# Kernel optimization log

Hardware: AMD Instinct MI355X
Metric: run time of the kernel (lower is better)

Reference implementation:

```python
import jax, jax.numpy as jnp
import numpy as np

MODEL_DIM = 1024
NUM_HEADS = 16
K_DIM = MODEL_DIM // NUM_HEADS


def setup_inputs() -> dict:
    key = jax.random.key(0)
    kx, kw1, kw2 = jax.random.split(key, 3)
    B, L, D = 4, 2048, MODEL_DIM
    x = jax.random.normal(kx, (B, L, D), dtype=jnp.float32)
    # nn.Linear(D, 3D, bias=False): y = x @ W^T; store transposed form [D, 3D]
    scale1 = 1.0 / np.sqrt(D)
    Wqkv = jax.random.uniform(kw1, (D, 3 * D), dtype=jnp.float32, minval=-scale1, maxval=scale1)
    Wout = jax.random.uniform(kw2, (D, D), dtype=jnp.float32, minval=-scale1, maxval=scale1)
    return {"x": x, "Wqkv": Wqkv, "Wout": Wout}


def reference(x, Wqkv, Wout):
    B, L, D = x.shape
    H, Kd = NUM_HEADS, K_DIM
    qkv = x @ Wqkv  # [B, L, 3D]
    q, k, v = jnp.split(qkv, 3, axis=-1)

    def heads(t):  # [B, L, D] -> [B, H, L, Kd]
        return t.reshape(B, L, H, Kd).transpose(0, 2, 1, 3)

    qh, kh, vh = heads(q), heads(k), heads(v)
    scores = jnp.einsum('bhqd,bhkd->bhqk', qh, kh) / jnp.sqrt(jnp.float32(Kd))
    causal = jnp.triu(jnp.ones((L, L), dtype=bool), k=1)  # True above diagonal
    scores = jnp.where(causal, -jnp.inf, scores)
    probs = jax.nn.softmax(scores, axis=-1)
    attended = jnp.einsum('bhqk,bhkd->bhqd', probs, vh)
    concatted = attended.transpose(0, 2, 1, 3).reshape(B, L, D)
    # dropout is identity in eval mode
    return concatted @ Wout
```

## Files before the change

kernel.cpp:

```cpp
#include <hip/hip_runtime.h>

typedef unsigned short u16;
typedef unsigned int   u32;
typedef __bf16   bf16x8 __attribute__((ext_vector_type(8)));
typedef float    f32x4  __attribute__((ext_vector_type(4)));
typedef u16      u16x4  __attribute__((ext_vector_type(4)));
typedef u16      u16x8  __attribute__((ext_vector_type(8)));
typedef u32      u32x2  __attribute__((ext_vector_type(2)));
typedef u32      u32x4  __attribute__((ext_vector_type(4)));

#if __has_builtin(__builtin_amdgcn_exp2f)
#define EXP2(x) __builtin_amdgcn_exp2f(x)
#else
#define EXP2(x) exp2f(x)
#endif

__device__ __forceinline__ u16 f2bf(float f) {
    unsigned u = __float_as_uint(f);
    u += 0x7FFFu + ((u >> 16) & 1u);
    return (u16)(u >> 16);
}

__device__ __forceinline__ u32 pack_bf16(float a, float b) {
#if __has_builtin(__builtin_amdgcn_cvt_pk_bf16_f32)
    typedef __bf16 bf16x2 __attribute__((ext_vector_type(2)));
    bf16x2 r = __builtin_amdgcn_cvt_pk_bf16_f32(a, b);
    return __builtin_bit_cast(u32, r);
#else
    return (u32)f2bf(a) | ((u32)f2bf(b) << 16);
#endif
}

__device__ __forceinline__ void async_copy16(const u16* g, u16* l) {
    __builtin_amdgcn_global_load_lds(
        (const __attribute__((address_space(1))) unsigned*)g,
        (__attribute__((address_space(3))) unsigned*)l, 16, 0, 0);
}

__device__ __forceinline__ bf16x8 lds_frag(const u16* p) {
    return *(const bf16x8*)p;
}

__device__ __forceinline__ void permlane32_swap(u32& a, u32& b) {
    asm("v_permlane32_swap_b32 %0, %1" : "+v"(a), "+v"(b));
}
__device__ __forceinline__ void permlane16_swap(u32& a, u32& b) {
    asm("v_permlane16_swap_b32 %0, %1" : "+v"(a), "+v"(b));
}

__global__ __launch_bounds__(256) void prep(const float* __restrict__ x,
                                            const float* __restrict__ Wqkv,
                                            const float* __restrict__ Wout,
                                            u16* __restrict__ xb,
                                            u16* __restrict__ wqkv_t,
                                            u16* __restrict__ wout_t) {
    __shared__ u16 t[64 * 72];
    const int bid = blockIdx.x;
    const int tid = threadIdx.x;

    if (bid >= 1024) {
        size_t i = ((size_t)(bid - 1024) * 256 + tid) * 8;
        float4 v0 = *(const float4*)(x + i);
        float4 v1 = *(const float4*)(x + i + 4);
        u16x8 o = { f2bf(v0.x), f2bf(v0.y), f2bf(v0.z), f2bf(v0.w),
                    f2bf(v1.x), f2bf(v1.y), f2bf(v1.z), f2bf(v1.w) };
        *(u16x8*)(xb + i) = o;
        return;
    }

    const float* W;  u16* Wt;  int Kd, Nd, n0, k0;
    if (bid < 768) { W = Wqkv; Wt = wqkv_t; Kd = 1024; Nd = 3072;
                     n0 = (bid % 48) * 64; k0 = (bid / 48) * 64; }
    else           { W = Wout; Wt = wout_t; Kd = 1024; Nd = 1024;
                     n0 = ((bid - 768) % 16) * 64; k0 = ((bid - 768) / 16) * 64; }
#pragma unroll
    for (int i = 0; i < 4; ++i) {
        int lin = i * 256 + tid;
        int kr = lin >> 4, nc = (lin & 15) << 2;
        float4 v = *(const float4*)(W + (size_t)(k0 + kr) * Nd + n0 + nc);
        u16x4 o = { f2bf(v.x), f2bf(v.y), f2bf(v.z), f2bf(v.w) };
        *(u16x4*)&t[kr * 72 + nc] = o;
    }
    __syncthreads();
#pragma unroll
    for (int i = 0; i < 2; ++i) {
        int lin = i * 256 + tid;
        int nr = lin >> 3, kc = (lin & 7) << 3;
        u16x8 o;
#pragma unroll
        for (int jj = 0; jj < 8; ++jj) o[jj] = t[(kc + jj) * 72 + nr];
        *(u16x8*)(Wt + (size_t)(n0 + nr) * Kd + k0 + kc) = o;
    }
}

__global__ __launch_bounds__(256) void gemm_qkv(const u16* __restrict__ A,
                                                const u16* __restrict__ Bt,
                                                u16* __restrict__ outb,
                                                int K, int N) {
    __shared__ u16 As[2][128 * 32];
    __shared__ u16 Bs[2][128 * 32];
    const int tid = threadIdx.x;
    const int lane = tid & 63;
    const int wv = tid >> 6;
    const int wr = (wv >> 1) * 64;
    const int wc = (wv & 1) * 64;
    const int qd = lane >> 4;
    const int c  = lane & 15;
    const int m0 = blockIdx.y * 128;
    const int n0 = blockIdx.x * 128;

    const int srow = tid >> 2;
    const int sg = ((tid & 3) ^ ((srow >> 1) & 3)) << 3;

    const u16* Ag0 = A  + (size_t)(m0 +      srow) * K + sg;
    const u16* Ag1 = A  + (size_t)(m0 + 64 + srow) * K + sg;
    const u16* Bg0 = Bt + (size_t)(n0 +      srow) * K + sg;
    const u16* Bg1 = Bt + (size_t)(n0 + 64 + srow) * K + sg;

    const u32 fsw = (qd ^ ((c >> 1) & 3)) << 3;
    const u32 a_off = (wr + c) * 32 + fsw;
    const u32 b_off = (wc + c) * 32 + fsw;

    f32x4 acc[4][4] = {};

    async_copy16(Ag0, &As[0][tid * 8]);
    async_copy16(Ag1, &As[0][2048 + tid * 8]);
    async_copy16(Bg0, &Bs[0][tid * 8]);
    async_copy16(Bg1, &Bs[0][2048 + tid * 8]);

    int p = 0;
    for (int k0 = 0; k0 < K; k0 += 32) {
        __syncthreads();
        if (k0 + 32 < K) {
            const int np = p ^ 1;
            async_copy16(Ag0 + k0 + 32, &As[np][tid * 8]);
            async_copy16(Ag1 + k0 + 32, &As[np][2048 + tid * 8]);
            async_copy16(Bg0 + k0 + 32, &Bs[np][tid * 8]);
            async_copy16(Bg1 + k0 + 32, &Bs[np][2048 + tid * 8]);
        }
        bf16x8 af[4], bfr[4];
#pragma unroll
        for (int i = 0; i < 4; ++i) af[i]  = lds_frag(&As[p][a_off + i * 512]);
#pragma unroll
        for (int j = 0; j < 4; ++j) bfr[j] = lds_frag(&Bs[p][b_off + j * 512]);
#pragma unroll
        for (int i = 0; i < 4; ++i)
#pragma unroll
            for (int j = 0; j < 4; ++j)
                acc[i][j] = __builtin_amdgcn_mfma_f32_16x16x32_bf16(af[i], bfr[j], acc[i][j], 0, 0, 0);
        p ^= 1;
    }

#pragma unroll
    for (int i = 0; i < 4; ++i)
#pragma unroll
        for (int j = 0; j < 4; ++j) {
            int n = n0 + wc + j * 16 + c;
            int which = n >> 10, h = (n >> 6) & 15, kd = n & 63;
            int m_base = m0 + wr + i * 16 + qd * 4;
            int b = m_base >> 11, l0 = m_base & 2047;
            int bh = b * 16 + h;
            if (which == 2) {
                u32x2 o2;
                o2[0] = pack_bf16(acc[i][j][0], acc[i][j][1]);
                o2[1] = pack_bf16(acc[i][j][2], acc[i][j][3]);
                *(u32x2*)(outb + (size_t)(128 + bh) * 131072 + (size_t)kd * 2048 + l0) = o2;
            } else if (which == 0) {
#pragma unroll
                for (int r = 0; r < 4; ++r)
                    outb[(size_t)bh * 131072 + (size_t)(l0 + r) * 64 + kd] =
                        f2bf(acc[i][j][r] * 0.1803368801f);
            } else {
#pragma unroll
                for (int r = 0; r < 4; ++r)
                    outb[(size_t)(64 + bh) * 131072 + (size_t)(l0 + r) * 64 + kd] =
                        f2bf(acc[i][j][r]);
            }
        }
}

__global__ __launch_bounds__(256) void gemm_out(const u16* __restrict__ A,
                                                const u16* __restrict__ Bt,
                                                float* __restrict__ outf,
                                                int K, int N) {
    __shared__ u16 As[2][64 * 32];
    __shared__ u16 Bs[2][128 * 32];
    const int tid = threadIdx.x;
    const int lane = tid & 63;
    const int wv = tid >> 6;
    const int wr = (wv >> 1) * 32;
    const int wc = (wv & 1) * 64;
    const int qd = lane >> 4;
    const int c  = lane & 15;
    const int m0 = blockIdx.y * 64;
    const int n0 = blockIdx.x * 128;

    const int srow = tid >> 2;
    const int sg = ((tid & 3) ^ ((srow >> 1) & 3)) << 3;

    const u16* Ag0 = A  + (size_t)(m0 +      srow) * K + sg;
    const u16* Bg0 = Bt + (size_t)(n0 +      srow) * K + sg;
    const u16* Bg1 = Bt + (size_t)(n0 + 64 + srow) * K + sg;

    const u32 fsw = (qd ^ ((c >> 1) & 3)) << 3;
    const u32 a_off = (wr + c) * 32 + fsw;
    const u32 b_off = (wc + c) * 32 + fsw;

    f32x4 acc[2][4] = {};

    async_copy16(Ag0, &As[0][tid * 8]);
    async_copy16(Bg0, &Bs[0][tid * 8]);
    async_copy16(Bg1, &Bs[0][2048 + tid * 8]);

    int p = 0;
    for (int k0 = 0; k0 < K; k0 += 32) {
        __syncthreads();
        if (k0 + 32 < K) {
            const int np = p ^ 1;
            async_copy16(Ag0 + k0 + 32, &As[np][tid * 8]);
            async_copy16(Bg0 + k0 + 32, &Bs[np][tid * 8]);
            async_copy16(Bg1 + k0 + 32, &Bs[np][2048 + tid * 8]);
        }
        bf16x8 af[2], bfr[4];
#pragma unroll
        for (int i = 0; i < 2; ++i) af[i]  = lds_frag(&As[p][a_off + i * 512]);
#pragma unroll
        for (int j = 0; j < 4; ++j) bfr[j] = lds_frag(&Bs[p][b_off + j * 512]);
#pragma unroll
        for (int i = 0; i < 2; ++i)
#pragma unroll
            for (int j = 0; j < 4; ++j)
                acc[i][j] = __builtin_amdgcn_mfma_f32_16x16x32_bf16(af[i], bfr[j], acc[i][j], 0, 0, 0);
        p ^= 1;
    }

#pragma unroll
    for (int i = 0; i < 2; ++i)
#pragma unroll
        for (int j = 0; j < 4; ++j)
#pragma unroll
            for (int r = 0; r < 4; ++r) {
                int m = m0 + wr + i * 16 + qd * 4 + r;
                int n = n0 + wc + j * 16 + c;
                outf[(size_t)m * N + n] = acc[i][j][r];
            }
}

#define ATTN_S_AB(KSB)                                                        \
    do {                                                                      \
        _Pragma("unroll") for (int f = 0; f < 8; ++f) {                       \
            sa[f] = f32x4{-8.f, -8.f, -8.f, -8.f};                            \
            sb[f] = f32x4{-8.f, -8.f, -8.f, -8.f};                            \
        }                                                                     \
        __builtin_amdgcn_s_setprio(1);                                        \
        _Pragma("unroll") for (int ks = 0; ks < 2; ++ks) {                    \
            const u16* kp = (KSB) + kf_off[ks];                               \
            _Pragma("unroll") for (int f = 0; f < 8; ++f) {                   \
                bf16x8 kf = lds_frag(kp + f * 1024);                          \
                sa[f] = __builtin_amdgcn_mfma_f32_16x16x32_bf16(              \
                    kf, qa[ks], sa[f], 0, 0, 0);                              \
                sb[f] = __builtin_amdgcn_mfma_f32_16x16x32_bf16(              \
                    kf, qb[ks], sb[f], 0, 0, 0);                              \
            }                                                                 \
        }                                                                     \
        __builtin_amdgcn_s_setprio(0);                                        \
    } while (0)

#define ATTN_FINISH_AB(VTB, KT)                                               \
    do {                                                                      \
        if ((KT) == qt) {                                                     \
            _Pragma("unroll") for (int f = 0; f < 8; ++f)                     \
                _Pragma("unroll") for (int r = 0; r < 4; ++r) {               \
                    int key = (KT) * 128 + f * 16 + qd * 4 + r;               \
                    if (key > qa_row) sa[f][r] = -3e38f;                      \
                    if (key > qb_row) sb[f][r] = -3e38f;                      \
                }                                                             \
        }                                                                     \
        _Pragma("unroll") for (int f = 0; f < 8; ++f) {                       \
            _Pragma("unroll") for (int r = 0; r < 4; ++r) {                   \
                sa[f][r] = EXP2(sa[f][r]);                                    \
                sb[f][r] = EXP2(sb[f][r]);                                    \
            }                                                                 \
            rva += sa[f];                                                     \
            rvb += sb[f];                                                     \
        }                                                                     \
        _Pragma("unroll") for (int kc = 0; kc < 4; ++kc) {                    \
            u32 a0 = pack_bf16(sa[2 * kc][0], sa[2 * kc][1]);                 \
            u32 a1 = pack_bf16(sa[2 * kc + 1][0], sa[2 * kc + 1][1]);         \
            u32 b0 = pack_bf16(sa[2 * kc][2], sa[2 * kc][3]);                 \
            u32 b1 = pack_bf16(sa[2 * kc + 1][2], sa[2 * kc + 1][3]);         \
            permlane32_swap(a0, a1); permlane16_swap(a0, a1);                 \
            permlane32_swap(b0, b1); permlane16_swap(b0, b1);                 \
            u32x4 wpa = {a0, b0, a1, b1};                                     \
            bf16x8 pa = __builtin_bit_cast(bf16x8, wpa);                      \
            u32 c0 = pack_bf16(sb[2 * kc][0], sb[2 * kc][1]);                 \
            u32 c1 = pack_bf16(sb[2 * kc + 1][0], sb[2 * kc + 1][1]);         \
            u32 d0 = pack_bf16(sb[2 * kc][2], sb[2 * kc][3]);                 \
            u32 d1 = pack_bf16(sb[2 * kc + 1][2], sb[2 * kc + 1][3]);         \
            permlane32_swap(c0, c1); permlane16_swap(c0, c1);                 \
            permlane32_swap(d0, d1); permlane16_swap(d0, d1);                 \
            u32x4 wpb = {c0, d0, c1, d1};                                     \
            bf16x8 pb = __builtin_bit_cast(bf16x8, wpb);                      \
            const u16* vp = (VTB) + vf_off[kc];                               \
            __builtin_amdgcn_s_setprio(1);                                    \
            _Pragma("unroll") for (int jo = 0; jo < 4; ++jo) {                \
                bf16x8 vf = lds_frag(vp + jo * 2048);                         \
                acca[jo] = __builtin_amdgcn_mfma_f32_16x16x32_bf16(           \
                    vf, pa, acca[jo], 0, 0, 0);                               \
                accb[jo] = __builtin_amdgcn_mfma_f32_16x16x32_bf16(           \
                    vf, pb, accb[jo], 0, 0, 0);                               \
            }                                                                 \
            __builtin_amdgcn_s_setprio(0);                                    \
        }                                                                     \
    } while (0)

__global__ __launch_bounds__(256, 2) void attn_kernel(const u16* __restrict__ qkv,
                                                      u16* __restrict__ att) {
    __shared__ u16 Ks[2][128 * 64];
    __shared__ u16 Vt[2][64 * 128];

    const int tid = threadIdx.x;
    const int lane = tid & 63;
    const int w = tid >> 6;
    const int qd = lane >> 4;
    const int c = lane & 15;

    const int flat = blockIdx.x + 8 * blockIdx.y;
    const int bh = (flat & 7) + 8 * ((flat >> 3) & 7);
    const int bx = flat >> 6;
    const int b = bh >> 4, h = bh & 15;

    const u16* Qg = qkv + (size_t)bh * 131072;
    const u16* Kg = qkv + (size_t)(64 + bh) * 131072;
    const u16* Vg = qkv + (size_t)(128 + bh) * 131072;

    u32 kf_off[2];
#pragma unroll
    for (int ks = 0; ks < 2; ++ks)
        kf_off[ks] = c * 64 + (((ks * 4 + qd) ^ (c & 7)) << 3);
    u32 vf_off[4];
#pragma unroll
    for (int kc = 0; kc < 4; ++kc)
        vf_off[kc] = c * 128 + (((kc * 4 + qd) ^ c) << 3);

    auto issue_copy = [&](int t, u16* kd, u16* vd) {
#pragma unroll
        for (int it = 0; it < 4; ++it) {
            int lin = it * 256 + tid;
            int krw = lin >> 3, kch = lin & 7;
            int vrw = lin >> 4, vch = lin & 15;
            async_copy16(Kg + (size_t)t * 8192 + krw * 64 + ((kch ^ (krw & 7)) << 3),
                         kd + lin * 8);
            async_copy16(Vg + (size_t)t * 128 + (size_t)vrw * 2048 + ((vch ^ (vrw & 15)) << 3),
                         vd + lin * 8);
        }
    };

#pragma unroll 1
    for (int seg = 0; seg < 2; ++seg) {
        const int qt = seg ? (15 - bx) : bx;
        const int qa_row = qt * 128 + w * 32 + c;
        const int qb_row = qa_row + 16;

        bf16x8 qa[2], qb[2];
#pragma unroll
        for (int ks = 0; ks < 2; ++ks) {
            qa[ks] = *(const bf16x8*)(Qg + (size_t)qa_row * 64 + ks * 32 + qd * 8);
            qb[ks] = *(const bf16x8*)(Qg + (size_t)qb_row * 64 + ks * 32 + qd * 8);
        }

        f32x4 acca[4] = {}, accb[4] = {};
        f32x4 rva = {}, rvb = {};
        f32x4 sa[8], sb[8];

        const int nkt = qt + 1;

        __syncthreads();
        issue_copy(0, Ks[0], Vt[0]);
        __syncthreads();
        if (nkt > 1) issue_copy(1, Ks[1], Vt[1]);

#pragma unroll 1
        for (int kt = 0; kt < nkt; ++kt) {
            const int p = kt & 1;
            ATTN_S_AB(Ks[p]);
            ATTN_FINISH_AB(Vt[p], kt);
            if (kt + 1 < nkt) {
                __syncthreads();
                if (kt + 2 < nkt) issue_copy(kt + 2, Ks[p], Vt[p]);
            }
        }

        float ra = rva[0] + rva[1] + rva[2] + rva[3];
        float rb = rvb[0] + rvb[1] + rvb[2] + rvb[3];
        ra += __shfl_xor(ra, 16, 64);
        ra += __shfl_xor(ra, 32, 64);
        rb += __shfl_xor(rb, 16, 64);
        rb += __shfl_xor(rb, 32, 64);
        float ia = __builtin_amdgcn_rcpf(ra), ib = __builtin_amdgcn_rcpf(rb);
        u16* ar = att + ((size_t)b * 2048 + qa_row) * 1024 + h * 64;
        u16* br = att + ((size_t)b * 2048 + qb_row) * 1024 + h * 64;
#pragma unroll
        for (int jo = 0; jo < 4; ++jo) {
            u32x2 oa, ob;
            oa[0] = pack_bf16(acca[jo][0] * ia, acca[jo][1] * ia);
            oa[1] = pack_bf16(acca[jo][2] * ia, acca[jo][3] * ia);
            ob[0] = pack_bf16(accb[jo][0] * ib, accb[jo][1] * ib);
            ob[1] = pack_bf16(accb[jo][2] * ib, accb[jo][3] * ib);
            *(u32x2*)(ar + jo * 16 + qd * 4) = oa;
            *(u32x2*)(br + jo * 16 + qd * 4) = ob;
        }
    }
}

extern "C" void kernel_launch(void* const* d_in, const int* in_sizes, int n_in,
                              void* d_out, int out_size, void* d_ws, size_t ws_size,
                              hipStream_t stream) {
    const float* x    = (const float*)d_in[0];
    const float* Wqkv = (const float*)d_in[1];
    const float* Wout = (const float*)d_in[2];
    float* out = (float*)d_out;

    char* ws = (char*)d_ws;
    u16* x_bf   = (u16*)(ws);
    u16* wqkv_t = (u16*)(ws + 16777216);
    u16* wout_t = (u16*)(ws + 23068672);
    u16* qkv_h  = (u16*)(ws + 25165824);
    u16* att    = (u16*)(ws + 75497472);

    prep<<<dim3(5120), dim3(256), 0, stream>>>(x, Wqkv, Wout, x_bf, wqkv_t, wout_t);
    gemm_qkv<<<dim3(24, 64), dim3(256), 0, stream>>>(x_bf, wqkv_t, qkv_h, 1024, 3072);
    attn_kernel<<<dim3(8, 64), dim3(256), 0, stream>>>(qkv_h, att);
    gemm_out<<<dim3(8, 128), dim3(256), 0, stream>>>(att, wout_t, out, 1024, 1024);
}
```

Baseline: 246.2 us.

## Enlarge QKV GEMM to 256x256 tiles with 8 waves and swizzled block order

Rewrites the QKV projection GEMM to use 256x256 output tiles with 512 threads (8 waves), a BK of 64 with a double-buffered LDS ring, and explicit waitcnt/barrier scheduling with setprio around the MFMA clusters. The block index is remapped so that consecutive blocks share input tiles in the L2 cache. The aim is more data reuse per loaded tile and better overlap of global loads with MFMA work. In exchange it uses much more LDS (128KB) and more accumulator registers, which lowers occupancy and leaves only 384 blocks to spread over the CUs.

```diff
diff --git a/kernel.cpp b/kernel.cpp
--- a/kernel.cpp
+++ b/kernel.cpp
@@ -93,71 +93,136 @@
     }
 }
 
-__global__ __launch_bounds__(256) void gemm_qkv(const u16* __restrict__ A,
+__global__ __launch_bounds__(512) void gemm_qkv(const u16* __restrict__ A,
                                                 const u16* __restrict__ Bt,
                                                 u16* __restrict__ outb,
                                                 int K, int N) {
-    __shared__ u16 As[2][128 * 32];
-    __shared__ u16 Bs[2][128 * 32];
+    __shared__ u16 As[2][2][128 * 64];
+    __shared__ u16 Bs[2][2][128 * 64];
+
     const int tid = threadIdx.x;
     const int lane = tid & 63;
-    const int wv = tid >> 6;
-    const int wr = (wv >> 1) * 64;
-    const int wc = (wv & 1) * 64;
+    const int wid = tid >> 6;
+    const int wr = wid >> 2;
+    const int wc = wid & 3;
     const int qd = lane >> 4;
     const int c  = lane & 15;
-    const int m0 = blockIdx.y * 128;
-    const int n0 = blockIdx.x * 128;
-
-    const int srow = tid >> 2;
-    const int sg = ((tid & 3) ^ ((srow >> 1) & 3)) << 3;
-
-    const u16* Ag0 = A  + (size_t)(m0 +      srow) * K + sg;
-    const u16* Ag1 = A  + (size_t)(m0 + 64 + srow) * K + sg;
-    const u16* Bg0 = Bt + (size_t)(n0 +      srow) * K + sg;
-    const u16* Bg1 = Bt + (size_t)(n0 + 64 + srow) * K + sg;
-
-    const u32 fsw = (qd ^ ((c >> 1) & 3)) << 3;
-    const u32 a_off = (wr + c) * 32 + fsw;
-    const u32 b_off = (wc + c) * 32 + fsw;
-
-    f32x4 acc[4][4] = {};
-
-    async_copy16(Ag0, &As[0][tid * 8]);
-    async_copy16(Ag1, &As[0][2048 + tid * 8]);
-    async_copy16(Bg0, &Bs[0][tid * 8]);
-    async_copy16(Bg1, &Bs[0][2048 + tid * 8]);
-
-    int p = 0;
-    for (int k0 = 0; k0 < K; k0 += 32) {
-        __syncthreads();
-        if (k0 + 32 < K) {
-            const int np = p ^ 1;
-            async_copy16(Ag0 + k0 + 32, &As[np][tid * 8]);
-            async_copy16(Ag1 + k0 + 32, &As[np][2048 + tid * 8]);
-            async_copy16(Bg0 + k0 + 32, &Bs[np][tid * 8]);
-            async_copy16(Bg1 + k0 + 32, &Bs[np][2048 + tid * 8]);
-        }
+
+    const int flat = blockIdx.x;
+    const int swz  = (flat & 7) * 48 + (flat >> 3);
+    const int m0 = (swz / 12) * 256;
+    const int n0 = (swz % 12) * 256;
+
+    const u32 ch0 = (u32)((qd ^ (c & 7)) << 3);
+    const u32 ch1 = (u32)(((4 + qd) ^ (c & 7)) << 3);
+    const u32 arow = (u32)c * 64;
+    const u32 brow = ((u32)((wc & 1) * 64) + (u32)c) * 64;
+
+    auto stage = [&](int t, int slot) {
+        const int kb = t * 64;
+#pragma unroll
+        for (int it = 0; it < 4; ++it) {
+            int lin = it * 512 + tid;
+            int row = lin >> 3;
+            int sch = ((lin & 7) ^ (row & 7)) << 3;
+            async_copy16(A  + (size_t)(m0 + row) * K + kb + sch,
+                         &As[slot][0][0] + (size_t)lin * 8);
+            async_copy16(Bt + (size_t)(n0 + row) * K + kb + sch,
+                         &Bs[slot][0][0] + (size_t)lin * 8);
+        }
+    };
+
+    f32x4 acc[8][4] = {};
+
+    stage(0, 0);
+    stage(1, 1);
+    asm volatile("s_waitcnt vmcnt(8)" ::: "memory");
+    __builtin_amdgcn_s_barrier();
+
+    const int NT = K >> 6;
+#pragma unroll 1
+    for (int kt = 0; kt < NT; ++kt) {
+        const int p = kt & 1;
+        const u16* Ab = &As[p][wr][0];
+        const u16* Bb = &Bs[p][wc >> 1][0];
+
         bf16x8 af[4], bfr[4];
-#pragma unroll
-        for (int i = 0; i < 4; ++i) af[i]  = lds_frag(&As[p][a_off + i * 512]);
-#pragma unroll
-        for (int j = 0; j < 4; ++j) bfr[j] = lds_frag(&Bs[p][b_off + j * 512]);
+
+#pragma unroll
+        for (int i = 0; i < 4; ++i) af[i]  = lds_frag(Ab + arow + i * 1024 + ch0);
+#pragma unroll
+        for (int j = 0; j < 4; ++j) bfr[j] = lds_frag(Bb + brow + j * 1024 + ch0);
+        __builtin_amdgcn_s_barrier();
+        asm volatile("s_waitcnt lgkmcnt(0)" ::: "memory");
+        __builtin_amdgcn_sched_barrier(0);
+        __builtin_amdgcn_s_setprio(1);
 #pragma unroll
         for (int i = 0; i < 4; ++i)
 #pragma unroll
             for (int j = 0; j < 4; ++j)
                 acc[i][j] = __builtin_amdgcn_mfma_f32_16x16x32_bf16(af[i], bfr[j], acc[i][j], 0, 0, 0);
-        p ^= 1;
+        __builtin_amdgcn_s_setprio(0);
+        __builtin_amdgcn_s_barrier();
+
+#pragma unroll
+        for (int i = 0; i < 4; ++i) af[i] = lds_frag(Ab + arow + (4 + i) * 1024 + ch0);
+        __builtin_amdgcn_s_barrier();
+        asm volatile("s_waitcnt lgkmcnt(0)" ::: "memory");
+        __builtin_amdgcn_sched_barrier(0);
+        __builtin_amdgcn_s_setprio(1);
+#pragma unroll
+        for (int i = 0; i < 4; ++i)
+#pragma unroll
+            for (int j = 0; j < 4; ++j)
+                acc[4 + i][j] = __builtin_amdgcn_mfma_f32_16x16x32_bf16(af[i], bfr[j], acc[4 + i][j], 0, 0, 0);
+        __builtin_amdgcn_s_setprio(0);
+        __builtin_amdgcn_s_barrier();
+
+#pragma unroll
+        for (int i = 0; i < 4; ++i) af[i]  = lds_frag(Ab + arow + i * 1024 + ch1);
+#pragma unroll
+        for (int j = 0; j < 4; ++j) bfr[j] = lds_frag(Bb + brow + j * 1024 + ch1);
+        __builtin_amdgcn_s_barrier();
+        asm volatile("s_waitcnt lgkmcnt(0)" ::: "memory");
+        __builtin_amdgcn_sched_barrier(0);
+        __builtin_amdgcn_s_setprio(1);
+#pragma unroll
+        for (int i = 0; i < 4; ++i)
+#pragma unroll
+            for (int j = 0; j < 4; ++j)
+                acc[i][j] = __builtin_amdgcn_mfma_f32_16x16x32_bf16(af[i], bfr[j], acc[i][j], 0, 0, 0);
+        __builtin_amdgcn_s_setprio(0);
+        __builtin_amdgcn_s_barrier();
+
+#pragma unroll
+        for (int i = 0; i < 4; ++i) af[i] = lds_frag(Ab + arow + (4 + i) * 1024 + ch1);
+        __builtin_amdgcn_s_barrier();
+        asm volatile("s_waitcnt lgkmcnt(0)" ::: "memory");
+        __builtin_amdgcn_sched_barrier(0);
+        __builtin_amdgcn_s_setprio(1);
+#pragma unroll
+        for (int i = 0; i < 4; ++i)
+#pragma unroll
+            for (int j = 0; j < 4; ++j)
+                acc[4 + i][j] = __builtin_amdgcn_mfma_f32_16x16x32_bf16(af[i], bfr[j], acc[4 + i][j], 0, 0, 0);
+        __builtin_amdgcn_s_setprio(0);
+        __builtin_amdgcn_s_barrier();
+
+        if (kt + 2 < NT) stage(kt + 2, p);
+        if (kt + 1 < NT) {
+            if (kt + 2 < NT) asm volatile("s_waitcnt vmcnt(8)" ::: "memory");
+            else             asm volatile("s_waitcnt vmcnt(0)" ::: "memory");
+            __builtin_amdgcn_s_barrier();
+        }
     }
 
 #pragma unroll
-    for (int i = 0; i < 4; ++i)
+    for (int i = 0; i < 8; ++i)
 #pragma unroll
         for (int j = 0; j < 4; ++j) {
-            int n = n0 + wc + j * 16 + c;
+            int n = n0 + wc * 64 + j * 16 + c;
             int which = n >> 10, h = (n >> 6) & 15, kd = n & 63;
-            int m_base = m0 + wr + i * 16 + qd * 4;
+            int m_base = m0 + wr * 128 + i * 16 + qd * 4;
             int b = m_base >> 11, l0 = m_base & 2047;
             int bh = b * 16 + h;
             if (which == 2) {
@@ -429,7 +494,7 @@
     u16* att    = (u16*)(ws + 75497472);
 
     prep<<<dim3(5120), dim3(256), 0, stream>>>(x, Wqkv, Wout, x_bf, wqkv_t, wout_t);
-    gemm_qkv<<<dim3(24, 64), dim3(256), 0, stream>>>(x_bf, wqkv_t, qkv_h, 1024, 3072);
+    gemm_qkv<<<dim3(384), dim3(512), 0, stream>>>(x_bf, wqkv_t, qkv_h, 1024, 3072);
     attn_kernel<<<dim3(8, 64), dim3(256), 0, stream>>>(qkv_h, att);
     gemm_out<<<dim3(8, 128), dim3(256), 0, stream>>>(att, wout_t, out, 1024, 1024);
 }
```

Result: slower. 264.1 us (+7.3%).
